# Kernel tuning notes

Measured on AMD Instinct MI355X. Metric: run time of the kernel, lower is better.

The kernel has to match this reference:

```python
import jax, jax.numpy as jnp
import numpy as np

IN_SIZE = 256
OUT_SIZE = 256
WIN = 2  # window_size


def setup_inputs() -> dict:
    key = jax.random.key(0)
    k1, k2 = jax.random.split(key)
    x = jax.random.normal(k1, (8, 4096, IN_SIZE), dtype=jnp.float32)
    W = jax.random.normal(k2, (3 * OUT_SIZE, WIN * IN_SIZE), dtype=jnp.float32) * 0.05
    b = jnp.zeros((3 * OUT_SIZE,), dtype=jnp.float32)
    return {"x": x, "W": W, "b": b}


def reference(x, W, b):
    bsz, seq_len, _ = x.shape
    toks = [x]
    for i in range(WIN - 1):
        shifted = jnp.concatenate(
            [jnp.zeros((bsz, i + 1, IN_SIZE), x.dtype), x[:, : -(i + 1), :]], axis=1
        )
        toks.insert(0, shifted)
    xw = jnp.stack(toks, axis=2).reshape(bsz, seq_len, WIN * IN_SIZE)

    # Gated projection: z (update), f (forget), o (output)
    y = xw @ W.T + b  # (B, S, 3*OUT)
    z, f, o = jnp.split(y, 3, axis=2)
    z = jnp.tanh(z)
    f = jax.nn.sigmoid(f)

    # fo-pooling recurrence: c_t = f_t * c_{t-1} + (1 - f_t) * z_t
    def step(c, fz):
        ft, zt = fz
        c = ft * c + (1.0 - ft) * zt
        return c, c

    fz = (jnp.swapaxes(f, 0, 1), jnp.swapaxes(z, 0, 1))  # (S, B, OUT)
    c0 = jnp.zeros((bsz, OUT_SIZE), z.dtype)
    _, cs = jax.lax.scan(step, c0, fz)
    c = jnp.swapaxes(cs, 0, 1)  # (B, S, OUT)

    return jax.nn.sigmoid(o) * c
```

## Files before the change

kernel.cpp:

```cpp
#include <hip/hip_runtime.h>
#include <cstdint>
#include <cstddef>

#define BATCH  8
#define SEQ    4096
#define CHN    256
#define NQ     768
#define KTOT   512
#define S_B    64
#define TS     128
#define NCHUNK (SEQ/TS)

#define WPLANE 12320
#define WBUF   (4*WPLANE)

typedef __attribute__((ext_vector_type(8))) __bf16    bf16x8;
typedef __attribute__((ext_vector_type(4))) __bf16    bf16x4;
typedef __attribute__((ext_vector_type(4))) float     f32x4;
typedef __attribute__((ext_vector_type(4))) _Float16  f16x4;
typedef __attribute__((ext_vector_type(2))) _Float16  f16x2;

__global__ __launch_bounds__(256) void k_convW(const float* __restrict__ W,
                                               __bf16* __restrict__ Wt) {
    int lin = blockIdx.x * 256 + threadIdx.x;
    int n  = lin % NQ;
    int tg = lin / NQ;
    const float* src = W + (size_t)n * KTOT + tg * 8;
    float4 a = *(const float4*)(src);
    float4 b = *(const float4*)(src + 4);
    bf16x8 h;
    h[0]=(__bf16)a.x; h[1]=(__bf16)a.y; h[2]=(__bf16)a.z; h[3]=(__bf16)a.w;
    h[4]=(__bf16)b.x; h[5]=(__bf16)b.y; h[6]=(__bf16)b.z; h[7]=(__bf16)b.w;
    *(bf16x8*)(Wt + (size_t)lin * 8) = h;
}

__device__ __forceinline__ float fast_sigmoid(float y) {
    float e = __expf(-y);
    return __builtin_amdgcn_rcpf(1.f + e);
}
__device__ __forceinline__ float fast_tanh(float y) {
    float e = __expf(-2.f * y);
    return __builtin_amdgcn_rcpf(1.f + e) * 2.f - 1.f;
}

__global__ __launch_bounds__(768, 3) void k_gemm(
    const float* __restrict__ x, const __bf16* __restrict__ Wt,
    const float* __restrict__ bias,
    _Float16* __restrict__ Zb, _Float16* __restrict__ Fb, _Float16* __restrict__ Ob)
{
    __shared__ char As_b[(S_B + 1) * 512];
    __shared__ char Wl_b[2][WBUF];

    int tid = threadIdx.x;
    int bi  = blockIdx.x >> 6;
    int sc  = blockIdx.x & 63;
    int s0  = sc * S_B;
    int wid = tid >> 6;
    int l   = tid & 63;
    int l15 = l & 15, lg = l >> 4;

    #pragma unroll
    for (int i = 0; i < 6; ++i) {
        int idx = tid + i * 768;
        if (idx < (S_B + 1) * 64) {
            int r  = idx >> 6, cg = idx & 63;
            int srow = s0 - 1 + r;
            float4 v = make_float4(0.f, 0.f, 0.f, 0.f);
            if (srow >= 0)
                v = *(const float4*)(x + ((size_t)bi * SEQ + srow) * CHN + cg * 4);
            bf16x4 h;
            h[0]=(__bf16)v.x; h[1]=(__bf16)v.y; h[2]=(__bf16)v.z; h[3]=(__bf16)v.w;
            int boff = (r * 512 + cg * 8) ^ ((r & 7) << 4);
            *(bf16x4*)(As_b + boff) = h;
        }
    }

    const char* wt_lane = (const char*)Wt + ((size_t)wid * 64 + l) * 16;
    #define STAGE_W(bufi, t)                                                     \
        {                                                                        \
            _Pragma("unroll")                                                    \
            for (int g = 0; g < 4; ++g) {                                        \
                const char* gsrc = wt_lane + (size_t)(t) * 49152 + g * 12288;    \
                char* ldst = Wl_b[bufi] + g * WPLANE + wid * 1024;               \
                __builtin_amdgcn_global_load_lds(                                \
                    (const __attribute__((address_space(1))) void*)gsrc,         \
                    (__attribute__((address_space(3))) void*)ldst, 16, 0, 0);    \
            }                                                                    \
        }

    STAGE_W(0, 0);
    __syncthreads();

    f32x4 acc[4][4];
    const f32x4 vzero = {0.f, 0.f, 0.f, 0.f};
    #pragma unroll
    for (int a = 0; a < 4; ++a)
        #pragma unroll
        for (int b = 0; b < 4; ++b)
            acc[a][b] = vzero;

    #pragma unroll
    for (int t = 0; t < 16; ++t) {
        if (t < 15) STAGE_W((t + 1) & 1, t + 1);

        int kh  = t >> 3;
        int kc0 = (t & 7) * 32;
        bf16x8 xf[4];
        #pragma unroll
        for (int st = 0; st < 4; ++st) {
            int row  = st * 16 + l15 + kh;
            int boff = (row * 512 + kc0 * 2 + lg * 16) ^ ((row & 7) << 4);
            xf[st] = *(const bf16x8*)(As_b + boff);
        }
        bf16x8 wf[4];
        #pragma unroll
        for (int nt = 0; nt < 4; ++nt)
            wf[nt] = *(const bf16x8*)(Wl_b[t & 1] + lg * WPLANE +
                                      (wid * 64 + nt * 16 + l15) * 16);

        __builtin_amdgcn_s_setprio(1);
        #pragma unroll
        for (int nt = 0; nt < 4; ++nt)
            #pragma unroll
            for (int st = 0; st < 4; ++st)
                acc[nt][st] = __builtin_amdgcn_mfma_f32_16x16x32_bf16(
                                  wf[nt], xf[st], acc[nt][st], 0, 0, 0);
        __builtin_amdgcn_s_setprio(0);

        if (t < 15) __syncthreads();
    }

    int gate = wid >> 2;
    _Float16* buf = (gate == 0) ? Zb : (gate == 1) ? Fb : Ob;
    bool is_tanh = (gate == 0);
    #pragma unroll
    for (int nt = 0; nt < 4; ++nt) {
        int n4  = wid * 64 + nt * 16 + lg * 4;
        int chn = n4 & 255;
        float4 bv = *(const float4*)(bias + n4);
        #pragma unroll
        for (int st = 0; st < 4; ++st) {
            int s = s0 + st * 16 + l15;
            f16x4 h;
            #pragma unroll
            for (int r = 0; r < 4; ++r) {
                float bvr = (r == 0) ? bv.x : (r == 1) ? bv.y : (r == 2) ? bv.z : bv.w;
                float y = acc[nt][st][r] + bvr;
                float v = is_tanh ? fast_tanh(y) : fast_sigmoid(y);
                h[r] = (_Float16)v;
            }
            *(f16x4*)(buf + ((size_t)bi * SEQ + s) * CHN + chn) = h;
        }
    }
}

__global__ __launch_bounds__(128) void k_scan1(const _Float16* __restrict__ Fb,
                                               const _Float16* __restrict__ Zb,
                                               float* __restrict__ Aq,
                                               float* __restrict__ Bq) {
    int bi = blockIdx.x >> 5;
    int ck = blockIdx.x & 31;
    int c2 = threadIdx.x;
    size_t base = (((size_t)bi * SEQ + ck * TS) * CHN + c2 * 2) >> 1;
    const f16x2* F2 = (const f16x2*)Fb;
    const f16x2* Z2 = (const f16x2*)Zb;
    float a0 = 1.f, a1 = 1.f, c0 = 0.f, c1 = 0.f;
    #pragma unroll 8
    for (int s = 0; s < TS; ++s) {
        f16x2 f = F2[base + (size_t)s * (CHN / 2)];
        f16x2 z = Z2[base + (size_t)s * (CHN / 2)];
        float f0 = (float)f[0], f1 = (float)f[1];
        c0 = f0 * c0 + (1.f - f0) * (float)z[0];
        c1 = f1 * c1 + (1.f - f1) * (float)z[1];
        a0 *= f0; a1 *= f1;
    }
    int o = blockIdx.x * CHN + c2 * 2;
    *(float2*)(Aq + o) = make_float2(a0, a1);
    *(float2*)(Bq + o) = make_float2(c0, c1);
}

__global__ __launch_bounds__(256) void k_scan2(const float* __restrict__ Aq,
                                               const float* __restrict__ Bq,
                                               float* __restrict__ Cq) {
    int bi = blockIdx.x;
    int ch = threadIdx.x;
    float c = 0.f;
    #pragma unroll
    for (int ck = 0; ck < NCHUNK; ++ck) {
        int o = (bi * NCHUNK + ck) * CHN + ch;
        Cq[o] = c;
        c = Aq[o] * c + Bq[o];
    }
}

__global__ __launch_bounds__(128) void k_scan3(const _Float16* __restrict__ Fb,
                                               const _Float16* __restrict__ Zb,
                                               const _Float16* __restrict__ Ob,
                                               const float* __restrict__ Cq,
                                               float* __restrict__ out) {
    int bi = blockIdx.x >> 5;
    int ck = blockIdx.x & 31;
    int c2 = threadIdx.x;
    float2 c = *(const float2*)(Cq + blockIdx.x * CHN + c2 * 2);
    size_t base = (((size_t)bi * SEQ + ck * TS) * CHN + c2 * 2) >> 1;
    const f16x2* F2 = (const f16x2*)Fb;
    const f16x2* Z2 = (const f16x2*)Zb;
    const f16x2* O2 = (const f16x2*)Ob;
    float* outp = out + (((size_t)bi * SEQ + ck * TS) * CHN + c2 * 2);
    #pragma unroll 4
    for (int s = 0; s < TS; ++s) {
        f16x2 f  = F2[base + (size_t)s * (CHN / 2)];
        f16x2 z  = Z2[base + (size_t)s * (CHN / 2)];
        f16x2 so = O2[base + (size_t)s * (CHN / 2)];
        float f0 = (float)f[0], f1 = (float)f[1];
        c.x = f0 * c.x + (1.f - f0) * (float)z[0];
        c.y = f1 * c.y + (1.f - f1) * (float)z[1];
        *(float2*)(outp + (size_t)s * CHN) = make_float2((float)so[0] * c.x,
                                                         (float)so[1] * c.y);
    }
}

extern "C" void kernel_launch(void* const* d_in, const int* in_sizes, int n_in,
                              void* d_out, int out_size, void* d_ws, size_t ws_size,
                              hipStream_t stream)
{
    const float* x = (const float*)d_in[0];
    const float* W = (const float*)d_in[1];
    const float* b = (const float*)d_in[2];
    float* out = (float*)d_out;

    char* ws = (char*)d_ws;
    const size_t MB = 1024 * 1024;
    _Float16* Zb = (_Float16*)(ws +  0 * MB);
    _Float16* Fb = (_Float16*)(ws + 16 * MB);
    _Float16* Ob = (_Float16*)(ws + 32 * MB);
    __bf16*   Wt = (__bf16*)  (ws + 48 * MB);
    float*    Aq = (float*)   (ws + 49 * MB);
    float*    Bq = (float*)   (ws + 50 * MB);
    float*    Cq = (float*)   (ws + 51 * MB);

    k_convW<<<dim3(192),            dim3(256), 0, stream>>>(W, Wt);
    k_gemm <<<dim3(BATCH * 64),     dim3(768), 0, stream>>>(x, Wt, b, Zb, Fb, Ob);
    k_scan1<<<dim3(BATCH * NCHUNK), dim3(128), 0, stream>>>(Fb, Zb, Aq, Bq);
    k_scan2<<<dim3(BATCH),          dim3(256), 0, stream>>>(Aq, Bq, Cq);
    k_scan3<<<dim3(BATCH * NCHUNK), dim3(128), 0, stream>>>(Fb, Zb, Ob, Cq, out);
}
```

Baseline: 88.23 us.

## Split GEMM blocks by gate slice into three 256-thread blocks per tile

The GEMM kernel now launches three times as many blocks, each with 256 threads handling one of the z/f/o output slices (256 columns), instead of one 768-thread block covering all 768 columns. The weight staging layout in LDS shrinks accordingly, which lowers per-block LDS and raises the number of blocks that can be resident. The cost is that each block reconverts and reloads the same x tile into LDS, so x global reads and bf16 conversion work triple.

After: 97.77 us. 1.11x slower.

```diff
diff --git a/kernel.cpp b/kernel.cpp
--- a/kernel.cpp
+++ b/kernel.cpp
@@ -11,8 +11,8 @@
 #define TS     128
 #define NCHUNK (SEQ/TS)
 
-#define WPLANE 12320
-#define WBUF   (4*WPLANE)
+#define WPL    4128
+#define WBUF   (4*WPL)
 
 typedef __attribute__((ext_vector_type(8))) __bf16    bf16x8;
 typedef __attribute__((ext_vector_type(4))) __bf16    bf16x4;
@@ -43,7 +43,7 @@
     return __builtin_amdgcn_rcpf(1.f + e) * 2.f - 1.f;
 }
 
-__global__ __launch_bounds__(768, 3) void k_gemm(
+__global__ __launch_bounds__(256, 2) void k_gemm(
     const float* __restrict__ x, const __bf16* __restrict__ Wt,
     const float* __restrict__ bias,
     _Float16* __restrict__ Zb, _Float16* __restrict__ Fb, _Float16* __restrict__ Ob)
@@ -52,16 +52,19 @@
     __shared__ char Wl_b[2][WBUF];
 
     int tid = threadIdx.x;
-    int bi  = blockIdx.x >> 6;
-    int sc  = blockIdx.x & 63;
-    int s0  = sc * S_B;
-    int wid = tid >> 6;
+    int bid = blockIdx.x;
+    int nsl  = bid % 3;
+    int rest = bid / 3;
+    int bi = rest >> 6;
+    int sc = rest & 63;
+    int s0 = sc * S_B;
+    int wn  = tid >> 6;
     int l   = tid & 63;
     int l15 = l & 15, lg = l >> 4;
 
     #pragma unroll
-    for (int i = 0; i < 6; ++i) {
-        int idx = tid + i * 768;
+    for (int i = 0; i < 17; ++i) {
+        int idx = tid + i * 256;
         if (idx < (S_B + 1) * 64) {
             int r  = idx >> 6, cg = idx & 63;
             int srow = s0 - 1 + r;
@@ -75,13 +78,14 @@
         }
     }
 
-    const char* wt_lane = (const char*)Wt + ((size_t)wid * 64 + l) * 16;
+    const __bf16* wt_lane = Wt + ((size_t)nsl * 256 + l) * 8;
     #define STAGE_W(bufi, t)                                                     \
         {                                                                        \
             _Pragma("unroll")                                                    \
-            for (int g = 0; g < 4; ++g) {                                        \
-                const char* gsrc = wt_lane + (size_t)(t) * 49152 + g * 12288;    \
-                char* ldst = Wl_b[bufi] + g * WPLANE + wid * 1024;               \
+            for (int c = 0; c < 4; ++c) {                                        \
+                const __bf16* gsrc = wt_lane +                                   \
+                    ((size_t)((t) * 4 + wn) * NQ + c * 64) * 8;                  \
+                char* ldst = Wl_b[bufi] + wn * WPL + c * 1024;                   \
                 __builtin_amdgcn_global_load_lds(                                \
                     (const __attribute__((address_space(1))) void*)gsrc,         \
                     (__attribute__((address_space(3))) void*)ldst, 16, 0, 0);    \
@@ -115,8 +119,8 @@
         bf16x8 wf[4];
         #pragma unroll
         for (int nt = 0; nt < 4; ++nt)
-            wf[nt] = *(const bf16x8*)(Wl_b[t & 1] + lg * WPLANE +
-                                      (wid * 64 + nt * 16 + l15) * 16);
+            wf[nt] = *(const bf16x8*)(Wl_b[t & 1] + lg * WPL +
+                                      (wn * 64 + nt * 16 + l15) * 16);
 
         __builtin_amdgcn_s_setprio(1);
         #pragma unroll
@@ -130,14 +134,12 @@
         if (t < 15) __syncthreads();
     }
 
-    int gate = wid >> 2;
-    _Float16* buf = (gate == 0) ? Zb : (gate == 1) ? Fb : Ob;
-    bool is_tanh = (gate == 0);
+    _Float16* buf = (nsl == 0) ? Zb : (nsl == 1) ? Fb : Ob;
+    bool is_tanh = (nsl == 0);
     #pragma unroll
     for (int nt = 0; nt < 4; ++nt) {
-        int n4  = wid * 64 + nt * 16 + lg * 4;
-        int chn = n4 & 255;
-        float4 bv = *(const float4*)(bias + n4);
+        int chn = wn * 64 + nt * 16 + lg * 4;
+        float4 bv = *(const float4*)(bias + nsl * 256 + chn);
         #pragma unroll
         for (int st = 0; st < 4; ++st) {
             int s = s0 + st * 16 + l15;
@@ -240,7 +242,7 @@
     float*    Cq = (float*)   (ws + 51 * MB);
 
     k_convW<<<dim3(192),            dim3(256), 0, stream>>>(W, Wt);
-    k_gemm <<<dim3(BATCH * 64),     dim3(768), 0, stream>>>(x, Wt, b, Zb, Fb, Ob);
+    k_gemm <<<dim3(3 * BATCH * 64), dim3(256), 0, stream>>>(x, Wt, b, Zb, Fb, Ob);
     k_scan1<<<dim3(BATCH * NCHUNK), dim3(128), 0, stream>>>(Fb, Zb, Aq, Bq);
     k_scan2<<<dim3(BATCH),          dim3(256), 0, stream>>>(Aq, Bq, Cq);
     k_scan3<<<dim3(BATCH * NCHUNK), dim3(128), 0, stream>>>(Fb, Zb, Ob, Cq, out);
```

## Load GEMM weight fragments directly into registers with triple buffering

Applied to the files above, without the earlier changes.

Drops the LDS staging of bf16 weights via global_load_lds double buffering. Each lane now loads its weight fragments straight from global memory into registers, prefetched two k-steps ahead. This removes the per-iteration __syncthreads and about 98KB of LDS, which could raise occupancy. In exchange it adds vector registers and relies on L2/L1 hits for the weight reads, since lanes in different blocks re-read the same weights.

After: 74.02 us. 1.19x faster.

```diff
diff --git a/kernel.cpp b/kernel.cpp
--- a/kernel.cpp
+++ b/kernel.cpp
@@ -10,9 +10,6 @@
 #define S_B    64
 #define TS     128
 #define NCHUNK (SEQ/TS)
-
-#define WPLANE 12320
-#define WBUF   (4*WPLANE)
 
 typedef __attribute__((ext_vector_type(8))) __bf16    bf16x8;
 typedef __attribute__((ext_vector_type(4))) __bf16    bf16x4;
@@ -49,7 +46,6 @@
     _Float16* __restrict__ Zb, _Float16* __restrict__ Fb, _Float16* __restrict__ Ob)
 {
     __shared__ char As_b[(S_B + 1) * 512];
-    __shared__ char Wl_b[2][WBUF];
 
     int tid = threadIdx.x;
     int bi  = blockIdx.x >> 6;
@@ -75,21 +71,17 @@
         }
     }
 
-    const char* wt_lane = (const char*)Wt + ((size_t)wid * 64 + l) * 16;
-    #define STAGE_W(bufi, t)                                                     \
+    const __bf16* wp = Wt + ((size_t)lg * NQ + wid * 64 + l15) * 8;
+    #define LOADW(dst, t)                                                        \
         {                                                                        \
             _Pragma("unroll")                                                    \
-            for (int g = 0; g < 4; ++g) {                                        \
-                const char* gsrc = wt_lane + (size_t)(t) * 49152 + g * 12288;    \
-                char* ldst = Wl_b[bufi] + g * WPLANE + wid * 1024;               \
-                __builtin_amdgcn_global_load_lds(                                \
-                    (const __attribute__((address_space(1))) void*)gsrc,         \
-                    (__attribute__((address_space(3))) void*)ldst, 16, 0, 0);    \
-            }                                                                    \
-        }
-
-    STAGE_W(0, 0);
-    __syncthreads();
+            for (int nt = 0; nt < 4; ++nt)                                       \
+                dst[nt] = *(const bf16x8*)(wp + (size_t)(t) * 24576 + nt * 128); \
+        }
+
+    bf16x8 wf0[4], wf1[4], wf2[4];
+    LOADW(wf0, 0);
+    LOADW(wf1, 1);
 
     f32x4 acc[4][4];
     const f32x4 vzero = {0.f, 0.f, 0.f, 0.f};
@@ -99,9 +91,11 @@
         for (int b = 0; b < 4; ++b)
             acc[a][b] = vzero;
 
+    __syncthreads();
+
     #pragma unroll
     for (int t = 0; t < 16; ++t) {
-        if (t < 15) STAGE_W((t + 1) & 1, t + 1);
+        if (t < 14) LOADW(wf2, t + 2);
 
         int kh  = t >> 3;
         int kc0 = (t & 7) * 32;
@@ -112,11 +106,6 @@
             int boff = (row * 512 + kc0 * 2 + lg * 16) ^ ((row & 7) << 4);
             xf[st] = *(const bf16x8*)(As_b + boff);
         }
-        bf16x8 wf[4];
-        #pragma unroll
-        for (int nt = 0; nt < 4; ++nt)
-            wf[nt] = *(const bf16x8*)(Wl_b[t & 1] + lg * WPLANE +
-                                      (wid * 64 + nt * 16 + l15) * 16);
 
         __builtin_amdgcn_s_setprio(1);
         #pragma unroll
@@ -124,10 +113,11 @@
             #pragma unroll
             for (int st = 0; st < 4; ++st)
                 acc[nt][st] = __builtin_amdgcn_mfma_f32_16x16x32_bf16(
-                                  wf[nt], xf[st], acc[nt][st], 0, 0, 0);
+                                  wf0[nt], xf[st], acc[nt][st], 0, 0, 0);
         __builtin_amdgcn_s_setprio(0);
 
-        if (t < 15) __syncthreads();
+        #pragma unroll
+        for (int nt = 0; nt < 4; ++nt) { wf0[nt] = wf1[nt]; wf1[nt] = wf2[nt]; }
     }
 
     int gate = wid >> 2;
```
